# Performance work log

Hardware: AMD Instinct MI355X
Metric: run time of the kernel (lower is better)

## Reference

```python
import jax, jax.numpy as jnp
import numpy as np

N_NODES = 100000
DROPOUT_RATE = 0.1


def setup_inputs() -> dict:
    key = jax.random.key(0)
    k1, k2, k3, k4, k5 = jax.random.split(key, 5)
    N, E, DIN, DOUT = N_NODES, 3200000, 512, 256
    x = jax.random.normal(k1, (N, DIN), dtype=jnp.float32)
    # glorot-style weight
    limit = jnp.sqrt(6.0 / (DIN + DOUT)).astype(jnp.float32)
    W = jax.random.uniform(k2, (DIN, DOUT), dtype=jnp.float32, minval=-limit, maxval=limit)
    edge_src = jax.random.randint(k3, (E,), 0, N, dtype=jnp.int32)
    edge_dst = jax.random.randint(k4, (E,), 0, N, dtype=jnp.int32)
    edge_w = jax.random.uniform(k5, (E,), dtype=jnp.float32)
    return {"x": x, "W": W, "edge_src": edge_src, "edge_dst": edge_dst, "edge_w": edge_w}


def reference(x, W, edge_src, edge_dst, edge_w):
    # dropout (inverted scaling), deterministic mask from fixed key
    keep = 1.0 - DROPOUT_RATE
    mask = jax.random.bernoulli(jax.random.key(42), keep, x.shape)
    h = jnp.where(mask, x / keep, 0.0)
    # dense projection: [N, DIN] @ [DIN, DOUT]
    h = h @ W
    # sparse adjacency matmul: out[d] = sum_e w_e * h[src_e] for edges e with dst_e == d
    msgs = edge_w[:, None] * h[edge_src]              # [E, DOUT]
    agg = jax.ops.segment_sum(msgs, edge_dst, num_segments=N_NODES)  # [N, DOUT]
    return jax.nn.relu(agg)
```

## Files before the change

### kernel.cpp

```cpp
#include <hip/hip_runtime.h>
#include <stdint.h>

#define NNODES   100000
#define DIN      512
#define DOUT     256
#define BCAP     92

typedef short s16x4 __attribute__((ext_vector_type(4)));
typedef short s16x8 __attribute__((ext_vector_type(8)));
typedef float f32x4 __attribute__((ext_vector_type(4)));
typedef _Float16 f16x4 __attribute__((ext_vector_type(4)));

__device__ __forceinline__ void threefry_0_42(uint32_t c0, uint32_t c1,
                                              uint32_t& o0, uint32_t& o1) {
  const uint32_t ks0 = 0u, ks1 = 42u, ks2 = 0x1BD11BF0u;
  uint32_t x0 = c0 + ks0;
  uint32_t x1 = c1 + ks1;
#define TF_R(r) { x0 += x1; x1 = (x1 << (r)) | (x1 >> (32 - (r))); x1 ^= x0; }
  TF_R(13) TF_R(15) TF_R(26) TF_R(6)
  x0 += ks1; x1 += ks2 + 1u;
  TF_R(17) TF_R(29) TF_R(16) TF_R(24)
  x0 += ks2; x1 += ks0 + 2u;
  TF_R(13) TF_R(15) TF_R(26) TF_R(6)
  x0 += ks0; x1 += ks1 + 3u;
  TF_R(17) TF_R(29) TF_R(16) TF_R(24)
  x0 += ks1; x1 += ks2 + 4u;
  TF_R(13) TF_R(15) TF_R(26) TF_R(6)
  x0 += ks2; x1 += ks0 + 5u;
#undef TF_R
  o0 = x0; o1 = x1;
}

__device__ __forceinline__ float dropout_apply(float x, uint32_t idx) {
  uint32_t r0, r1;
  threefry_0_42(0u, idx, r0, r1);
  uint32_t bits = r0 ^ r1;
  float u = __uint_as_float((bits >> 9) | 0x3F800000u) - 1.0f;
  return (u < 0.9f) ? x * (1.0f / 0.9f) : 0.0f;
}

__device__ __forceinline__ ushort f2bf_rne(float f) {
  uint32_t u = __float_as_uint(f);
  uint32_t r = u + 0x7FFFu + ((u >> 16) & 1u);
  return (ushort)(r >> 16);
}
__device__ __forceinline__ float bf2f(ushort h) {
  return __uint_as_float(((uint32_t)h) << 16);
}

__launch_bounds__(256)
__global__ void w_split(const float* __restrict__ W,
                        ushort* __restrict__ WhT,
                        ushort* __restrict__ WlT) {
  __shared__ float T[64][65];
  const int t  = threadIdx.x;
  const int k0 = blockIdx.x * 64;
  const int c0 = blockIdx.y * 64;
#pragma unroll
  for (int i = 0; i < 4; ++i) {
    int q  = i * 256 + t;
    int kr = q >> 4;
    int c4 = (q & 15) * 4;
    float4 v = *(const float4*)(W + (size_t)(k0 + kr) * DOUT + c0 + c4);
    T[kr][c4 + 0] = v.x; T[kr][c4 + 1] = v.y;
    T[kr][c4 + 2] = v.z; T[kr][c4 + 3] = v.w;
  }
  __syncthreads();
#pragma unroll
  for (int i = 0; i < 2; ++i) {
    int q  = i * 256 + t;
    int c  = q >> 3;
    int k8 = (q & 7) * 8;
    s16x8 hv, lv;
#pragma unroll
    for (int j = 0; j < 8; ++j) {
      float f = T[k8 + j][c];
      ushort hh = f2bf_rne(f);
      hv[j] = (short)hh;
      lv[j] = (short)f2bf_rne(f - bf2f(hh));
    }
    size_t base = (size_t)(c0 + c) * DIN + (k0 + k8);
    *(s16x8*)(WhT + base) = hv;
    *(s16x8*)(WlT + base) = lv;
  }
}

__launch_bounds__(256, 4)
__global__ void mfma_dropout_gemm(const float* __restrict__ x,
                                  const ushort* __restrict__ WhT,
                                  const ushort* __restrict__ WlT,
                                  _Float16* __restrict__ h) {
  __shared__ ushort Ah[64 * 64];
  __shared__ ushort Al[64 * 64];

  const int tid  = threadIdx.x;
  const int lane = tid & 63;
  const int w    = tid >> 6;
  const int n0   = blockIdx.x * 64;
  const int lr   = lane & 15;
  const int lg   = lane >> 4;

  f32x4 acc[4][4];
#pragma unroll
  for (int mt = 0; mt < 4; ++mt)
#pragma unroll
    for (int nt = 0; nt < 4; ++nt)
      acc[mt][nt] = (f32x4){0.f, 0.f, 0.f, 0.f};

  for (int k0 = 0; k0 < DIN; k0 += 64) {
#pragma unroll
    for (int i = 0; i < 4; ++i) {
      int f  = i * 256 + tid;
      int r  = f >> 4;
      int k4 = (f & 15) << 2;
      int grow = n0 + r;
      float4 xv = make_float4(0.f, 0.f, 0.f, 0.f);
      if (grow < NNODES)
        xv = *(const float4*)(x + (size_t)grow * DIN + k0 + k4);
      uint32_t base = (uint32_t)grow * DIN + (uint32_t)(k0 + k4);
      float d0 = dropout_apply(xv.x, base + 0u);
      float d1 = dropout_apply(xv.y, base + 1u);
      float d2 = dropout_apply(xv.z, base + 2u);
      float d3 = dropout_apply(xv.w, base + 3u);
      s16x4 hv, lv;
      {
        ushort hh;
        hh = f2bf_rne(d0); hv[0] = (short)hh; lv[0] = (short)f2bf_rne(d0 - bf2f(hh));
        hh = f2bf_rne(d1); hv[1] = (short)hh; lv[1] = (short)f2bf_rne(d1 - bf2f(hh));
        hh = f2bf_rne(d2); hv[2] = (short)hh; lv[2] = (short)f2bf_rne(d2 - bf2f(hh));
        hh = f2bf_rne(d3); hv[3] = (short)hh; lv[3] = (short)f2bf_rne(d3 - bf2f(hh));
      }
      int elem = (r * 64 + k4) ^ ((r & 7) << 3);
      *(s16x4*)&Ah[elem] = hv;
      *(s16x4*)&Al[elem] = lv;
    }
    __syncthreads();

#pragma unroll
    for (int kk = 0; kk < 2; ++kk) {
      const int kb = kk * 32 + lg * 8;
      s16x8 a_h[4], a_l[4];
#pragma unroll
      for (int mt = 0; mt < 4; ++mt) {
        int r = mt * 16 + lr;
        int elem = (r * 64 + kb) ^ ((r & 7) << 3);
        a_h[mt] = *(const s16x8*)&Ah[elem];
        a_l[mt] = *(const s16x8*)&Al[elem];
      }
#pragma unroll
      for (int nt = 0; nt < 4; ++nt) {
        int c = w * 64 + nt * 16 + lr;
        size_t boff = (size_t)c * DIN + k0 + kb;
        s16x8 b_h = *(const s16x8*)(WhT + boff);
        s16x8 b_l = *(const s16x8*)(WlT + boff);
#pragma unroll
        for (int mt = 0; mt < 4; ++mt)
          acc[mt][nt] = __builtin_amdgcn_mfma_f32_16x16x32_bf16(a_h[mt], b_h, acc[mt][nt], 0, 0, 0);
#pragma unroll
        for (int mt = 0; mt < 4; ++mt)
          acc[mt][nt] = __builtin_amdgcn_mfma_f32_16x16x32_bf16(a_h[mt], b_l, acc[mt][nt], 0, 0, 0);
#pragma unroll
        for (int mt = 0; mt < 4; ++mt)
          acc[mt][nt] = __builtin_amdgcn_mfma_f32_16x16x32_bf16(a_l[mt], b_h, acc[mt][nt], 0, 0, 0);
      }
    }
    __syncthreads();
  }

#pragma unroll
  for (int mt = 0; mt < 4; ++mt) {
    int rbase = n0 + mt * 16 + lg * 4;
#pragma unroll
    for (int reg = 0; reg < 4; ++reg) {
      int row = rbase + reg;
      if (row < NNODES) {
#pragma unroll
        for (int nt = 0; nt < 4; ++nt) {
          int col = w * 64 + nt * 16 + lr;
          h[(size_t)row * DOUT + col] = (_Float16)acc[mt][nt][reg];
        }
      }
    }
  }
}

__launch_bounds__(256, 2)
__global__ void dropout_gemm_f32(const float* __restrict__ x,
                                 const float* __restrict__ W,
                                 float* __restrict__ h) {
  __shared__ float As[16][68];
  __shared__ float Bs[16][260];

  const int tid = threadIdx.x;
  const int n0  = blockIdx.x * 64;
  const int cg  = tid & 15;
  const int rg  = tid >> 4;
  const int arow = tid >> 2;
  const int ak4  = (tid & 3) << 2;
  const int bkk  = tid >> 4;

  float acc[4][16];
#pragma unroll
  for (int r = 0; r < 4; ++r)
#pragma unroll
    for (int c = 0; c < 16; ++c) acc[r][c] = 0.0f;

  for (int k0 = 0; k0 < DIN; k0 += 16) {
    {
      int n = n0 + arow;
      float4 xv = make_float4(0.f, 0.f, 0.f, 0.f);
      if (n < NNODES)
        xv = *(const float4*)(x + (size_t)n * DIN + k0 + ak4);
      uint32_t base = (uint32_t)n * DIN + (uint32_t)(k0 + ak4);
      As[ak4 + 0][arow] = dropout_apply(xv.x, base + 0u);
      As[ak4 + 1][arow] = dropout_apply(xv.y, base + 1u);
      As[ak4 + 2][arow] = dropout_apply(xv.z, base + 2u);
      As[ak4 + 3][arow] = dropout_apply(xv.w, base + 3u);
    }
    {
      const float* wrow = W + (size_t)(k0 + bkk) * DOUT + (cg << 2);
#pragma unroll
      for (int j4 = 0; j4 < 4; ++j4) {
        float4 wv = *(const float4*)(wrow + 64 * j4);
        *(float4*)&Bs[bkk][(cg << 2) + 64 * j4] = wv;
      }
    }
    __syncthreads();

#pragma unroll
    for (int kk = 0; kk < 16; ++kk) {
      float4 av  = *(const float4*)&As[kk][rg << 2];
      float4 bv0 = *(const float4*)&Bs[kk][(cg << 2) + 0];
      float4 bv1 = *(const float4*)&Bs[kk][(cg << 2) + 64];
      float4 bv2 = *(const float4*)&Bs[kk][(cg << 2) + 128];
      float4 bv3 = *(const float4*)&Bs[kk][(cg << 2) + 192];
      const float a[4]  = {av.x, av.y, av.z, av.w};
      const float b[16] = {bv0.x, bv0.y, bv0.z, bv0.w,
                           bv1.x, bv1.y, bv1.z, bv1.w,
                           bv2.x, bv2.y, bv2.z, bv2.w,
                           bv3.x, bv3.y, bv3.z, bv3.w};
#pragma unroll
      for (int r = 0; r < 4; ++r)
#pragma unroll
        for (int c = 0; c < 16; ++c) acc[r][c] = fmaf(a[r], b[c], acc[r][c]);
    }
    __syncthreads();
  }

#pragma unroll
  for (int rr = 0; rr < 4; ++rr) {
    int n = n0 + (rg << 2) + rr;
    if (n < NNODES) {
#pragma unroll
      for (int j4 = 0; j4 < 4; ++j4) {
        float4 v = make_float4(acc[rr][j4 * 4 + 0], acc[rr][j4 * 4 + 1],
                               acc[rr][j4 * 4 + 2], acc[rr][j4 * 4 + 3]);
        *(float4*)(h + (size_t)n * DOUT + (cg << 2) + 64 * j4) = v;
      }
    }
  }
}

__launch_bounds__(256)
__global__ void fill_buckets(const int* __restrict__ esrc, const int* __restrict__ edst,
                             const float* __restrict__ ew, int* __restrict__ counts,
                             int2* __restrict__ buckets, int E) {
  int e = blockIdx.x * blockDim.x + threadIdx.x;
  if (e < E) {
    int d = edst[e];
    int pos = atomicAdd(&counts[d], 1);
    if (pos < BCAP)
      buckets[(size_t)d * BCAP + pos] = make_int2(esrc[e], __float_as_int(ew[e]));
  }
}

__launch_bounds__(256)
__global__ void gather_reduce(const _Float16* __restrict__ h,
                              const int* __restrict__ counts,
                              const int2* __restrict__ buckets,
                              float* __restrict__ out) {
  const int wave = blockIdx.x * (blockDim.x >> 6) + (threadIdx.x >> 6);
  const int lane = threadIdx.x & 63;
  if (wave >= NNODES) return;
  int deg = counts[wave];
  deg = (deg > BCAP) ? BCAP : deg;
  const size_t base = (size_t)wave * BCAP;
  const int col = lane << 2;

  f32x4 a0 = {0.f, 0.f, 0.f, 0.f};
  f32x4 a1 = {0.f, 0.f, 0.f, 0.f};
  f32x4 a2 = {0.f, 0.f, 0.f, 0.f};
  f32x4 a3 = {0.f, 0.f, 0.f, 0.f};

  int j = 0;
  for (; j + 4 <= deg; j += 4) {
    int2 p0 = buckets[base + j + 0];
    int2 p1 = buckets[base + j + 1];
    int2 p2 = buckets[base + j + 2];
    int2 p3 = buckets[base + j + 3];
    f16x4 v0 = *(const f16x4*)(h + (size_t)(uint32_t)p0.x * DOUT + col);
    f16x4 v1 = *(const f16x4*)(h + (size_t)(uint32_t)p1.x * DOUT + col);
    f16x4 v2 = *(const f16x4*)(h + (size_t)(uint32_t)p2.x * DOUT + col);
    f16x4 v3 = *(const f16x4*)(h + (size_t)(uint32_t)p3.x * DOUT + col);
    float w0 = __int_as_float(p0.y);
    float w1 = __int_as_float(p1.y);
    float w2 = __int_as_float(p2.y);
    float w3 = __int_as_float(p3.y);
#pragma unroll
    for (int q = 0; q < 4; ++q) {
      a0[q] = fmaf(w0, (float)v0[q], a0[q]);
      a1[q] = fmaf(w1, (float)v1[q], a1[q]);
      a2[q] = fmaf(w2, (float)v2[q], a2[q]);
      a3[q] = fmaf(w3, (float)v3[q], a3[q]);
    }
  }
  for (; j < deg; ++j) {
    int2 p0 = buckets[base + j];
    f16x4 v0 = *(const f16x4*)(h + (size_t)(uint32_t)p0.x * DOUT + col);
    float w0 = __int_as_float(p0.y);
#pragma unroll
    for (int q = 0; q < 4; ++q) a0[q] = fmaf(w0, (float)v0[q], a0[q]);
  }

  f32x4 r;
#pragma unroll
  for (int q = 0; q < 4; ++q)
    r[q] = fmaxf((a0[q] + a1[q]) + (a2[q] + a3[q]), 0.f);
  *(f32x4*)(out + (size_t)wave * DOUT + col) = r;
}

__launch_bounds__(256)
__global__ void scatter_edges(const float* __restrict__ h,
                              const int* __restrict__ esrc,
                              const int* __restrict__ edst,
                              const float* __restrict__ ew,
                              float* __restrict__ out, int E) {
  const int lane   = threadIdx.x & 63;
  const int wave0  = (blockIdx.x * blockDim.x + threadIdx.x) >> 6;
  const int nwaves = (gridDim.x * blockDim.x) >> 6;
  for (int e = wave0; e < E; e += nwaves) {
    int s = esrc[e];
    int d = edst[e];
    float w = ew[e];
    float4 v = *(const float4*)(h + (size_t)s * DOUT + (lane << 2));
    float* o = out + (size_t)d * DOUT + (lane << 2);
    atomicAdd(o + 0, w * v.x);
    atomicAdd(o + 1, w * v.y);
    atomicAdd(o + 2, w * v.z);
    atomicAdd(o + 3, w * v.w);
  }
}

__launch_bounds__(256)
__global__ void relu_kernel(float* __restrict__ out, int n4) {
  int i = blockIdx.x * blockDim.x + threadIdx.x;
  if (i < n4) {
    float4 v = ((float4*)out)[i];
    v.x = fmaxf(v.x, 0.f);
    v.y = fmaxf(v.y, 0.f);
    v.z = fmaxf(v.z, 0.f);
    v.w = fmaxf(v.w, 0.f);
    ((float4*)out)[i] = v;
  }
}

extern "C" void kernel_launch(void* const* d_in, const int* in_sizes, int n_in,
                              void* d_out, int out_size, void* d_ws, size_t ws_size,
                              hipStream_t stream) {
  const float* x   = (const float*)d_in[0];
  const float* W   = (const float*)d_in[1];
  const int* esrc  = (const int*)d_in[2];
  const int* edst  = (const int*)d_in[3];
  const float* ew  = (const float*)d_in[4];
  float* out = (float*)d_out;
  const int E = in_sizes[2];

  const size_t h_bytes_f32 = (size_t)NNODES * DOUT * sizeof(float);
  const size_t cnt_bytes   = (size_t)NNODES * sizeof(int);
  const size_t cnt_pad     = (cnt_bytes + 255) & ~255ull;
  const size_t need        = h_bytes_f32 + 2 * cnt_pad + (size_t)E * sizeof(int2);

  char* ws = (char*)d_ws;
  const size_t h16_bytes  = (size_t)NNODES * DOUT * sizeof(_Float16);
  const size_t counts_off = h16_bytes;
  const size_t bkt_off    = counts_off + cnt_pad;
  const size_t bkt_bytes  = (size_t)NNODES * BCAP * sizeof(int2);
  const size_t wsp_off    = bkt_off + bkt_bytes;
  const size_t wsp_bytes  = (size_t)DOUT * DIN * sizeof(ushort);

  if (ws_size >= need) {
    _Float16* h16  = (_Float16*)(ws);
    int*  counts   = (int*)(ws + counts_off);
    int2* buckets  = (int2*)(ws + bkt_off);
    ushort* WhT    = (ushort*)(ws + wsp_off);
    ushort* WlT    = (ushort*)(ws + wsp_off + wsp_bytes);

    w_split<<<dim3(DIN / 64, DOUT / 64), 256, 0, stream>>>(W, WhT, WlT);
    mfma_dropout_gemm<<<(NNODES + 63) / 64, 256, 0, stream>>>(x, WhT, WlT, h16);

    hipMemsetAsync(counts, 0, cnt_bytes, stream);
    fill_buckets<<<(E + 255) / 256, 256, 0, stream>>>(esrc, edst, ew, counts, buckets, E);
    gather_reduce<<<(NNODES + 3) / 4, 256, 0, stream>>>(h16, counts, buckets, out);
  } else {
    float* h = (float*)(ws);
    dropout_gemm_f32<<<(NNODES + 63) / 64, 256, 0, stream>>>(x, W, h);
    hipMemsetAsync(d_out, 0, (size_t)out_size * sizeof(float), stream);
    scatter_edges<<<100000, 256, 0, stream>>>(h, esrc, edst, ew, out, E);
    int n4 = out_size / 4;
    relu_kernel<<<(n4 + 255) / 256, 256, 0, stream>>>(out, n4);
  }
}
```

Before: 1.004 ms.

## Stage W tiles in LDS, halve K-step, and coalesce output via LDS

The dropout GEMM kernel now loads the bf16 hi/lo W tiles into shared memory each K-step instead of having every wave read them straight from global memory. The K-tile shrinks from 64 to 32 so A and B fit together in a 40 KB LDS buffer, using a new swizzle. The fp16 output is first staged in LDS and then written as 16-byte row-contiguous stores instead of scattered 2-byte stores. The cost is twice as many K iterations and barriers, plus more LDS per block, which may lower occupancy.

Measured after the change: 1.011 ms. Within noise of the previous version (+0.7%).

```diff
diff --git a/kernel.cpp b/kernel.cpp
--- a/kernel.cpp
+++ b/kernel.cpp
@@ -85,13 +85,18 @@
   }
 }
 
+#define SWZA(r, k)  (((r) * 32 + (k)) ^ ((((r) >> 1) & 3) << 3))
+
 __launch_bounds__(256, 4)
 __global__ void mfma_dropout_gemm(const float* __restrict__ x,
                                   const ushort* __restrict__ WhT,
                                   const ushort* __restrict__ WlT,
                                   _Float16* __restrict__ h) {
-  __shared__ ushort Ah[64 * 64];
-  __shared__ ushort Al[64 * 64];
+  __shared__ ushort LB[20480];
+  ushort* Ah = LB;
+  ushort* Al = LB + 2048;
+  ushort* Bh = LB + 4096;
+  ushort* Bl = LB + 12288;
 
   const int tid  = threadIdx.x;
   const int lane = tid & 63;
@@ -99,6 +104,7 @@
   const int n0   = blockIdx.x * 64;
   const int lr   = lane & 15;
   const int lg   = lane >> 4;
+  const int kb   = lg * 8;
 
   f32x4 acc[4][4];
 #pragma unroll
@@ -107,12 +113,22 @@
     for (int nt = 0; nt < 4; ++nt)
       acc[mt][nt] = (f32x4){0.f, 0.f, 0.f, 0.f};
 
-  for (int k0 = 0; k0 < DIN; k0 += 64) {
+  for (int k0 = 0; k0 < DIN; k0 += 32) {
 #pragma unroll
     for (int i = 0; i < 4; ++i) {
+      int q  = i * 256 + tid;
+      int c  = q >> 2;
+      int k8 = (q & 3) << 3;
+      size_t src = (size_t)c * DIN + k0 + k8;
+      int elem = SWZA(c, k8);
+      *(s16x8*)&Bh[elem] = *(const s16x8*)(WhT + src);
+      *(s16x8*)&Bl[elem] = *(const s16x8*)(WlT + src);
+    }
+#pragma unroll
+    for (int i = 0; i < 2; ++i) {
       int f  = i * 256 + tid;
-      int r  = f >> 4;
-      int k4 = (f & 15) << 2;
+      int r  = f >> 3;
+      int k4 = (f & 7) << 2;
       int grow = n0 + r;
       float4 xv = make_float4(0.f, 0.f, 0.f, 0.f);
       if (grow < NNODES)
@@ -130,55 +146,62 @@
         hh = f2bf_rne(d2); hv[2] = (short)hh; lv[2] = (short)f2bf_rne(d2 - bf2f(hh));
         hh = f2bf_rne(d3); hv[3] = (short)hh; lv[3] = (short)f2bf_rne(d3 - bf2f(hh));
       }
-      int elem = (r * 64 + k4) ^ ((r & 7) << 3);
+      int elem = SWZA(r, k4);
       *(s16x4*)&Ah[elem] = hv;
       *(s16x4*)&Al[elem] = lv;
     }
     __syncthreads();
 
-#pragma unroll
-    for (int kk = 0; kk < 2; ++kk) {
-      const int kb = kk * 32 + lg * 8;
-      s16x8 a_h[4], a_l[4];
-#pragma unroll
-      for (int mt = 0; mt < 4; ++mt) {
-        int r = mt * 16 + lr;
-        int elem = (r * 64 + kb) ^ ((r & 7) << 3);
-        a_h[mt] = *(const s16x8*)&Ah[elem];
-        a_l[mt] = *(const s16x8*)&Al[elem];
-      }
-#pragma unroll
-      for (int nt = 0; nt < 4; ++nt) {
-        int c = w * 64 + nt * 16 + lr;
-        size_t boff = (size_t)c * DIN + k0 + kb;
-        s16x8 b_h = *(const s16x8*)(WhT + boff);
-        s16x8 b_l = *(const s16x8*)(WlT + boff);
-#pragma unroll
-        for (int mt = 0; mt < 4; ++mt)
-          acc[mt][nt] = __builtin_amdgcn_mfma_f32_16x16x32_bf16(a_h[mt], b_h, acc[mt][nt], 0, 0, 0);
-#pragma unroll
-        for (int mt = 0; mt < 4; ++mt)
-          acc[mt][nt] = __builtin_amdgcn_mfma_f32_16x16x32_bf16(a_h[mt], b_l, acc[mt][nt], 0, 0, 0);
-#pragma unroll
-        for (int mt = 0; mt < 4; ++mt)
-          acc[mt][nt] = __builtin_amdgcn_mfma_f32_16x16x32_bf16(a_l[mt], b_h, acc[mt][nt], 0, 0, 0);
-      }
+    s16x8 a_h[4], a_l[4];
+#pragma unroll
+    for (int mt = 0; mt < 4; ++mt) {
+      int r = mt * 16 + lr;
+      int elem = SWZA(r, kb);
+      a_h[mt] = *(const s16x8*)&Ah[elem];
+      a_l[mt] = *(const s16x8*)&Al[elem];
+    }
+#pragma unroll
+    for (int nt = 0; nt < 4; ++nt) {
+      int c = w * 64 + nt * 16 + lr;
+      int elem = SWZA(c, kb);
+      s16x8 b_h = *(const s16x8*)&Bh[elem];
+      s16x8 b_l = *(const s16x8*)&Bl[elem];
+#pragma unroll
+      for (int mt = 0; mt < 4; ++mt)
+        acc[mt][nt] = __builtin_amdgcn_mfma_f32_16x16x32_bf16(a_h[mt], b_h, acc[mt][nt], 0, 0, 0);
+#pragma unroll
+      for (int mt = 0; mt < 4; ++mt)
+        acc[mt][nt] = __builtin_amdgcn_mfma_f32_16x16x32_bf16(a_h[mt], b_l, acc[mt][nt], 0, 0, 0);
+#pragma unroll
+      for (int mt = 0; mt < 4; ++mt)
+        acc[mt][nt] = __builtin_amdgcn_mfma_f32_16x16x32_bf16(a_l[mt], b_h, acc[mt][nt], 0, 0, 0);
     }
     __syncthreads();
   }
 
-#pragma unroll
-  for (int mt = 0; mt < 4; ++mt) {
-    int rbase = n0 + mt * 16 + lg * 4;
-#pragma unroll
-    for (int reg = 0; reg < 4; ++reg) {
-      int row = rbase + reg;
-      if (row < NNODES) {
+  {
+    _Float16* C = (_Float16*)LB;
+#pragma unroll
+    for (int mt = 0; mt < 4; ++mt)
+#pragma unroll
+      for (int reg = 0; reg < 4; ++reg) {
+        int row = mt * 16 + lg * 4 + reg;
 #pragma unroll
         for (int nt = 0; nt < 4; ++nt) {
           int col = w * 64 + nt * 16 + lr;
-          h[(size_t)row * DOUT + col] = (_Float16)acc[mt][nt][reg];
+          C[row * 264 + col] = (_Float16)acc[mt][nt][reg];
         }
+      }
+    __syncthreads();
+#pragma unroll
+    for (int i = 0; i < 8; ++i) {
+      int q   = i * 256 + tid;
+      int row = q >> 5;
+      int ce  = (q & 31) << 3;
+      int grow = n0 + row;
+      if (grow < NNODES) {
+        s16x8 v = *(const s16x8*)((const ushort*)LB + row * 264 + ce);
+        *(s16x8*)((ushort*)h + (size_t)grow * DOUT + ce) = v;
       }
     }
   }
```
